# Performance work log

Hardware: AMD Instinct MI355X
Metric: run time of the kernel (lower is better)

## Reference

```python
import jax, jax.numpy as jnp
import numpy as np


def setup_inputs() -> dict:
    key = jax.random.key(0)
    kq, kk, kv = jax.random.split(key, 3)
    B, H, N, D = 4, 8, 2048, 64
    q = jax.random.normal(kq, (B, H, N, D), dtype=jnp.float32)
    k = jax.random.normal(kk, (B, H, N, D), dtype=jnp.float32)
    v = jax.random.normal(kv, (B, H, N, D), dtype=jnp.float32)
    return {"q": q, "k": k, "v": v}


def reference(q, k, v):
    # Naive attention exactly as the torch module: full [B,H,N,N] scores.
    scale = q.shape[-1] ** -0.5
    sim = jnp.einsum('bhid,bhjd->bhij', q, k) * scale  # [B,H,N,N]
    attn = jax.nn.softmax(sim, axis=-1)
    # dropout p=0.0 -> identity (module default; eval mode)
    out = jnp.einsum('bhij,bhjd->bhid', attn, v)  # [B,H,N,D]
    return out
```

## Files before the change

kernel.cpp:

```cpp
#include <hip/hip_runtime.h>

#define NN   2048
#define DD   64
#define KVB  32
#define NTW  16
#define BH   32
#define BHND (BH * NN * DD)
#define SC   0.18033688f
#define TSH  4096

typedef float    f32x4  __attribute__((ext_vector_type(4)));
typedef short    bf16x8 __attribute__((ext_vector_type(8)));
typedef unsigned u32x4  __attribute__((ext_vector_type(4)));

#define WAIT_VM4()   asm volatile("s_waitcnt vmcnt(4)" ::: "memory")
#define WAIT_VM0()   asm volatile("s_waitcnt vmcnt(0)" ::: "memory")
#define WAIT_LGKM0() asm volatile("s_waitcnt lgkmcnt(0)" ::: "memory")
#define SFENCE()     __builtin_amdgcn_sched_barrier(0)
#define SBAR()       __builtin_amdgcn_s_barrier()

__device__ __forceinline__ short f2bf(float x){
    unsigned u = __float_as_uint(x);
    u += 0x7FFF + ((u >> 16) & 1);
    return (short)(u >> 16);
}

__device__ __forceinline__ unsigned cvt_pk(float lo, float hi){
    unsigned r;
    asm("v_cvt_pk_bf16_f32 %0, %1, %2" : "=v"(r) : "v"(lo), "v"(hi));
    return r;
}

__device__ __forceinline__ float exp2_fast(float x){
    float r;
    asm("v_exp_f32 %0, %1" : "=v"(r) : "v"(x));
    return r;
}

__device__ __forceinline__ void gload_lds16(const short* g, short* l) {
    __builtin_amdgcn_global_load_lds(
        (const __attribute__((address_space(1))) void*)g,
        (__attribute__((address_space(3))) void*)l, 16, 0, 0);
}

__global__ __launch_bounds__(256)
void prep_frag(const float* __restrict__ k, const float* __restrict__ v,
               short* __restrict__ fr)
{
    const int tile = blockIdx.x;
    const int bh   = blockIdx.y;
    const int tid  = threadIdx.x;
    const int lane = tid & 63;
    const int f    = tid >> 6;
    const int l16  = lane & 15;
    const int lg   = lane >> 4;
    const long base = (long)bh * NN * DD;
    const int  kv0  = tile * KVB;
    short* tb = fr + ((long)bh * 64 + tile) * TSH;

    {
        const int cb = f >> 1, c = f & 1;
        const float* src = k + base + (long)(kv0 + cb * 16 + l16) * DD + c * 32 + lg * 8;
        f32x4 x0 = *(const f32x4*)src;
        f32x4 x1 = *(const f32x4*)(src + 4);
        bf16x8 o;
        #pragma unroll
        for (int j = 0; j < 4; ++j) { o[j] = f2bf(x0[j]); o[4 + j] = f2bf(x1[j]); }
        *(bf16x8*)(tb + (f * 64 + lane) * 8) = o;
    }
    {
        const float* vb = v + base;
        bf16x8 o;
        #pragma unroll
        for (int i = 0; i < 8; ++i) {
            float x = vb[(long)(kv0 + (i >> 2) * 16 + lg * 4 + (i & 3)) * DD + f * 16 + l16];
            o[i] = f2bf(x);
        }
        *(bf16x8*)(tb + 2048 + (f * 64 + lane) * 8) = o;
    }
}

__global__ __launch_bounds__(512, 2)
void attn_fwd_v19(const float* __restrict__ q,
                  const short* __restrict__ fr,
                  float* __restrict__ out)
{
    const int l     = blockIdx.x;
    const int xcd   = l & 7;
    const int idx   = l >> 3;
    const int qtile = idx & 15;
    const int bh    = xcd + 8 * (idx >> 4);

    const int tid   = threadIdx.x;
    const int wave  = tid >> 6;
    const int qg    = wave & 1;
    const int kvq   = wave >> 1;
    const int lane  = tid & 63;
    const int l16   = lane & 15;
    const int lg    = lane >> 4;

    __shared__ __align__(16) short lds_s[4][2][TSH];

    const long base  = (long)bh * NN * DD;
    const int  qrow0 = qtile * 128 + qg * 64;

    bf16x8 aq[4][2];
    #pragma unroll
    for (int j = 0; j < 4; ++j) {
        const float* qp = q + base + (long)(qrow0 + j * 16 + l16) * DD + lg * 8;
        #pragma unroll
        for (int c = 0; c < 2; ++c) {
            f32x4 x0 = *(const f32x4*)(qp + c * 32);
            f32x4 x1 = *(const f32x4*)(qp + c * 32 + 4);
            u32x4 pk;
            pk[0] = cvt_pk(x0[0] * SC, x0[1] * SC);
            pk[1] = cvt_pk(x0[2] * SC, x0[3] * SC);
            pk[2] = cvt_pk(x1[0] * SC, x1[1] * SC);
            pk[3] = cvt_pk(x1[2] * SC, x1[3] * SC);
            aq[j][c] = __builtin_bit_cast(bf16x8, pk);
        }
    }

    bf16x8 ones;
    #pragma unroll
    for (int i = 0; i < 8; ++i) ones[i] = (short)0x3F80;

    const short* fbase = fr + ((long)bh * 64 + kvq * NTW) * TSH + lane * 8;

    auto stage = [&](int buf, int tt) {
        const short* src = fbase + (long)tt * TSH + qg * 4 * 512;
        short* dst = &lds_s[kvq][buf][qg * 4 * 512];
        #pragma unroll
        for (int j = 0; j < 4; ++j)
            gload_lds16(src + j * 512, dst + j * 512);
    };

    f32x4 acc[4][4];
    f32x4 accS[4];
    #pragma unroll
    for (int t = 0; t < 4; ++t)
        #pragma unroll
        for (int j = 0; j < 4; ++j) acc[t][j] = f32x4{0.f, 0.f, 0.f, 0.f};
    #pragma unroll
    for (int j = 0; j < 4; ++j) accS[j] = f32x4{0.f, 0.f, 0.f, 0.f};

    stage(0, 0);
    stage(1, 1);

    for (int t = 0; t < NTW; ++t) {
        if (t == NTW - 1) { WAIT_VM0(); } else { WAIT_VM4(); }
        SFENCE();
        SBAR();

        const short* lb = &lds_s[kvq][t & 1][lane * 8];

        bf16x8 ka[2][2], bv[4];
        #pragma unroll
        for (int cb = 0; cb < 2; ++cb)
            #pragma unroll
            for (int c = 0; c < 2; ++c)
                ka[cb][c] = *(const bf16x8*)(lb + (cb * 2 + c) * 512);
        #pragma unroll
        for (int t2 = 0; t2 < 4; ++t2)
            bv[t2] = *(const bf16x8*)(lb + 2048 + t2 * 512);

        f32x4 s[2][4];
        __builtin_amdgcn_s_setprio(1);
        #pragma unroll
        for (int cb = 0; cb < 2; ++cb)
            #pragma unroll
            for (int j = 0; j < 4; ++j) {
                f32x4 z = f32x4{0.f, 0.f, 0.f, 0.f};
                z = __builtin_amdgcn_mfma_f32_16x16x32_bf16(ka[cb][0], aq[j][0], z, 0, 0, 0);
                z = __builtin_amdgcn_mfma_f32_16x16x32_bf16(ka[cb][1], aq[j][1], z, 0, 0, 0);
                s[cb][j] = z;
            }
        __builtin_amdgcn_s_setprio(0);

        SFENCE(); WAIT_LGKM0(); SFENCE();
        SBAR();
        if (t + 2 < NTW) stage(t & 1, t + 2);

        bf16x8 pa[4];
        #pragma unroll
        for (int j = 0; j < 4; ++j) {
            #pragma unroll
            for (int cb = 0; cb < 2; ++cb)
                #pragma unroll
                for (int r = 0; r < 4; ++r)
                    s[cb][j][r] = exp2_fast(s[cb][j][r]);
            u32x4 w;
            w[0] = cvt_pk(s[0][j][0], s[0][j][1]);
            w[1] = cvt_pk(s[0][j][2], s[0][j][3]);
            w[2] = cvt_pk(s[1][j][0], s[1][j][1]);
            w[3] = cvt_pk(s[1][j][2], s[1][j][3]);
            pa[j] = __builtin_bit_cast(bf16x8, w);
        }

        __builtin_amdgcn_s_setprio(1);
        #pragma unroll
        for (int t2 = 0; t2 < 4; ++t2)
            #pragma unroll
            for (int j = 0; j < 4; ++j)
                acc[t2][j] = __builtin_amdgcn_mfma_f32_16x16x32_bf16(pa[j], bv[t2], acc[t2][j], 0, 0, 0);
        #pragma unroll
        for (int j = 0; j < 4; ++j)
            accS[j] = __builtin_amdgcn_mfma_f32_16x16x32_bf16(pa[j], ones, accS[j], 0, 0, 0);
        __builtin_amdgcn_s_setprio(0);
    }

    __syncthreads();

    float* slot = (float*)&lds_s[0][0][0];
    #pragma unroll
    for (int r = 1; r <= 3; ++r) {
        if (kvq == r) {
            float* sp = slot + qg * 5120;
            #pragma unroll
            for (int t2 = 0; t2 < 4; ++t2)
                #pragma unroll
                for (int j = 0; j < 4; ++j)
                    *(f32x4*)&sp[((t2 * 4 + j) * 64 + lane) * 4] = acc[t2][j];
            #pragma unroll
            for (int j = 0; j < 4; ++j)
                *(f32x4*)&sp[((16 + j) * 64 + lane) * 4] = accS[j];
        }
        __syncthreads();
        if (kvq == 0) {
            const float* sp = slot + qg * 5120;
            #pragma unroll
            for (int t2 = 0; t2 < 4; ++t2)
                #pragma unroll
                for (int j = 0; j < 4; ++j)
                    acc[t2][j] += *(const f32x4*)&sp[((t2 * 4 + j) * 64 + lane) * 4];
            #pragma unroll
            for (int j = 0; j < 4; ++j)
                accS[j] += *(const f32x4*)&sp[((16 + j) * 64 + lane) * 4];
        }
        __syncthreads();
    }

    if (kvq == 0) {
        float* op = out + base + (long)qrow0 * DD;
        #pragma unroll
        for (int j = 0; j < 4; ++j) {
            f32x4 inv;
            #pragma unroll
            for (int r = 0; r < 4; ++r) inv[r] = 1.f / accS[j][r];
            #pragma unroll
            for (int t2 = 0; t2 < 4; ++t2)
                #pragma unroll
                for (int r = 0; r < 4; ++r)
                    op[(long)(j * 16 + lg * 4 + r) * DD + t2 * 16 + l16] = acc[t2][j][r] * inv[r];
        }
    }
}

extern "C" void kernel_launch(void* const* d_in, const int* in_sizes, int n_in,
                              void* d_out, int out_size, void* d_ws, size_t ws_size,
                              hipStream_t stream) {
    const float* q = (const float*)d_in[0];
    const float* k = (const float*)d_in[1];
    const float* v = (const float*)d_in[2];
    float* out = (float*)d_out;

    short* fr = (short*)d_ws;
    prep_frag<<<dim3(64, BH), 256, 0, stream>>>(k, v, fr);
    attn_fwd_v19<<<512, 512, 0, stream>>>(q, fr, out);
    (void)ws_size;
}
```

Before: 60.73 us.

## Drop shared-tile barriers: per-wave private K staging and direct V register loads

Blocks shrink from 8 waves (two q-groups sharing KV tiles) to 4 waves each owning a private KV slice and one 64-row q tile, with twice as many blocks. K fragments are double-buffered per wave in LDS with no block barriers in the loop. V fragments are now loaded from global memory straight into registers each step. This removes workgroup barriers and cross-wave LDS sharing, but KV data is fetched twice as often overall and the V loads put global latency directly in the loop.

```diff
diff --git a/kernel.cpp b/kernel.cpp
--- a/kernel.cpp
+++ b/kernel.cpp
@@ -14,10 +14,7 @@
 typedef unsigned u32x4  __attribute__((ext_vector_type(4)));
 
 #define WAIT_VM4()   asm volatile("s_waitcnt vmcnt(4)" ::: "memory")
-#define WAIT_VM0()   asm volatile("s_waitcnt vmcnt(0)" ::: "memory")
-#define WAIT_LGKM0() asm volatile("s_waitcnt lgkmcnt(0)" ::: "memory")
 #define SFENCE()     __builtin_amdgcn_sched_barrier(0)
-#define SBAR()       __builtin_amdgcn_s_barrier()
 
 __device__ __forceinline__ short f2bf(float x){
     unsigned u = __float_as_uint(x);
@@ -80,29 +77,27 @@
     }
 }
 
-__global__ __launch_bounds__(512, 2)
-void attn_fwd_v19(const float* __restrict__ q,
+__global__ __launch_bounds__(256, 2)
+void attn_fwd_v24(const float* __restrict__ q,
                   const short* __restrict__ fr,
                   float* __restrict__ out)
 {
     const int l     = blockIdx.x;
     const int xcd   = l & 7;
     const int idx   = l >> 3;
-    const int qtile = idx & 15;
-    const int bh    = xcd + 8 * (idx >> 4);
+    const int qtile = idx & 31;
+    const int bh    = xcd + 8 * (idx >> 5);
 
     const int tid   = threadIdx.x;
     const int wave  = tid >> 6;
-    const int qg    = wave & 1;
-    const int kvq   = wave >> 1;
     const int lane  = tid & 63;
     const int l16   = lane & 15;
     const int lg    = lane >> 4;
 
-    __shared__ __align__(16) short lds_s[4][2][TSH];
+    __shared__ __align__(16) short k_lds[4][2][2048];
 
     const long base  = (long)bh * NN * DD;
-    const int  qrow0 = qtile * 128 + qg * 64;
+    const int  qrow0 = qtile * 64;
 
     bf16x8 aq[4][2];
     #pragma unroll
@@ -123,13 +118,13 @@
 
     bf16x8 ones;
     #pragma unroll
-    for (int i = 0; i < 8; ++i) ones[i] = (short)0x3F80;
-
-    const short* fbase = fr + ((long)bh * 64 + kvq * NTW) * TSH + lane * 8;
-
-    auto stage = [&](int buf, int tt) {
-        const short* src = fbase + (long)tt * TSH + qg * 4 * 512;
-        short* dst = &lds_s[kvq][buf][qg * 4 * 512];
+    for (int ii = 0; ii < 8; ++ii) ones[ii] = (short)0x3F80;
+
+    const short* fbase = fr + ((long)bh * 64 + wave * NTW) * TSH + lane * 8;
+
+    auto stageK = [&](int buf, int tt) {
+        const short* src = fbase + (long)tt * TSH;
+        short* dst = &k_lds[wave][buf][0];
         #pragma unroll
         for (int j = 0; j < 4; ++j)
             gload_lds16(src + j * 512, dst + j * 512);
@@ -144,25 +139,25 @@
     #pragma unroll
     for (int j = 0; j < 4; ++j) accS[j] = f32x4{0.f, 0.f, 0.f, 0.f};
 
-    stage(0, 0);
-    stage(1, 1);
-
+    stageK(0, 0);
+
+    #pragma unroll 1
     for (int t = 0; t < NTW; ++t) {
-        if (t == NTW - 1) { WAIT_VM0(); } else { WAIT_VM4(); }
-        SFENCE();
-        SBAR();
-
-        const short* lb = &lds_s[kvq][t & 1][lane * 8];
-
-        bf16x8 ka[2][2], bv[4];
+        const short* vsrc = fbase + (long)t * TSH;
+        bf16x8 bvv[4];
+        #pragma unroll
+        for (int t2 = 0; t2 < 4; ++t2)
+            bvv[t2] = *(const bf16x8*)(vsrc + 2048 + t2 * 512);
+
+        SFENCE(); WAIT_VM4(); SFENCE();
+
+        const short* lb = &k_lds[wave][t & 1][lane * 8];
+        bf16x8 ka[2][2];
         #pragma unroll
         for (int cb = 0; cb < 2; ++cb)
             #pragma unroll
             for (int c = 0; c < 2; ++c)
                 ka[cb][c] = *(const bf16x8*)(lb + (cb * 2 + c) * 512);
-        #pragma unroll
-        for (int t2 = 0; t2 < 4; ++t2)
-            bv[t2] = *(const bf16x8*)(lb + 2048 + t2 * 512);
 
         f32x4 s[2][4];
         __builtin_amdgcn_s_setprio(1);
@@ -177,9 +172,7 @@
             }
         __builtin_amdgcn_s_setprio(0);
 
-        SFENCE(); WAIT_LGKM0(); SFENCE();
-        SBAR();
-        if (t + 2 < NTW) stage(t & 1, t + 2);
+        if (t + 1 < NTW) stageK((t + 1) & 1, t + 1);
 
         bf16x8 pa[4];
         #pragma unroll
@@ -202,7 +195,7 @@
         for (int t2 = 0; t2 < 4; ++t2)
             #pragma unroll
             for (int j = 0; j < 4; ++j)
-                acc[t2][j] = __builtin_amdgcn_mfma_f32_16x16x32_bf16(pa[j], bv[t2], acc[t2][j], 0, 0, 0);
+                acc[t2][j] = __builtin_amdgcn_mfma_f32_16x16x32_bf16(pa[j], bvv[t2], acc[t2][j], 0, 0, 0);
         #pragma unroll
         for (int j = 0; j < 4; ++j)
             accS[j] = __builtin_amdgcn_mfma_f32_16x16x32_bf16(pa[j], ones, accS[j], 0, 0, 0);
@@ -211,36 +204,34 @@
 
     __syncthreads();
 
-    float* slot = (float*)&lds_s[0][0][0];
+    float* slot = (float*)&k_lds[0][0][0];
     #pragma unroll
     for (int r = 1; r <= 3; ++r) {
-        if (kvq == r) {
-            float* sp = slot + qg * 5120;
+        if (wave == r) {
             #pragma unroll
             for (int t2 = 0; t2 < 4; ++t2)
                 #pragma unroll
                 for (int j = 0; j < 4; ++j)
-                    *(f32x4*)&sp[((t2 * 4 + j) * 64 + lane) * 4] = acc[t2][j];
+                    *(f32x4*)&slot[((t2 * 4 + j) * 64 + lane) * 4] = acc[t2][j];
             #pragma unroll
             for (int j = 0; j < 4; ++j)
-                *(f32x4*)&sp[((16 + j) * 64 + lane) * 4] = accS[j];
+                *(f32x4*)&slot[((16 + j) * 64 + lane) * 4] = accS[j];
         }
         __syncthreads();
-        if (kvq == 0) {
-            const float* sp = slot + qg * 5120;
+        if (wave == 0) {
             #pragma unroll
             for (int t2 = 0; t2 < 4; ++t2)
                 #pragma unroll
                 for (int j = 0; j < 4; ++j)
-                    acc[t2][j] += *(const f32x4*)&sp[((t2 * 4 + j) * 64 + lane) * 4];
+                    acc[t2][j] += *(const f32x4*)&slot[((t2 * 4 + j) * 64 + lane) * 4];
             #pragma unroll
             for (int j = 0; j < 4; ++j)
-                accS[j] += *(const f32x4*)&sp[((16 + j) * 64 + lane) * 4];
+                accS[j] += *(const f32x4*)&slot[((16 + j) * 64 + lane) * 4];
         }
         __syncthreads();
     }
 
-    if (kvq == 0) {
+    if (wave == 0) {
         float* op = out + base + (long)qrow0 * DD;
         #pragma unroll
         for (int j = 0; j < 4; ++j) {
@@ -266,6 +257,6 @@
 
     short* fr = (short*)d_ws;
     prep_frag<<<dim3(64, BH), 256, 0, stream>>>(k, v, fr);
-    attn_fwd_v19<<<512, 512, 0, stream>>>(q, fr, out);
+    attn_fwd_v24<<<1024, 256, 0, stream>>>(q, fr, out);
     (void)ws_size;
 }
```

New measurement: 57.76 us. 4.9% less time.
